# Optimization experiments

Hardware: AMD Instinct MI355X
Metric: run time of the kernel (lower is better)

## Reference

```python
import jax, jax.numpy as jnp
import numpy as np

EPS = 1e-5

def _conv1x1(x, w):
    # x: (B, Cin, N, K), w: (Cout, Cin) -> (B, Cout, N, K)
    return jnp.einsum('oc,bcnk->bonk', w, x)

def _bn2d(x, gamma, beta):
    # eval-mode BN with running_mean=0, running_var=1 (fresh init)
    scale = gamma / jnp.sqrt(1.0 + EPS)
    return x * scale[None, :, None, None] + beta[None, :, None, None]

def setup_inputs() -> dict:
    key = jax.random.key(0)
    ks = jax.random.split(key, 10)
    B, Cin, N, K = 8, 64, 1024, 32
    Cout, M = 64, 8
    Cin2 = 2 * Cin  # kernel_input='w_neighbor'
    features = jax.random.normal(ks[0], (B, Cin, N, K), dtype=jnp.float32)
    points_xyz = jax.random.normal(ks[1], (B, 3, N, K), dtype=jnp.float32)
    # ScoreNet convs: mlp_channels [7,16,16,16,M]; first 3 have BN (no bias), last has bias
    w1 = jax.random.normal(ks[2], (16, 7), dtype=jnp.float32) * (2.0 / 7) ** 0.5
    w2 = jax.random.normal(ks[3], (16, 16), dtype=jnp.float32) * (2.0 / 16) ** 0.5
    w3 = jax.random.normal(ks[4], (16, 16), dtype=jnp.float32) * (2.0 / 16) ** 0.5
    w4 = jax.random.normal(ks[5], (M, 16), dtype=jnp.float32) * (2.0 / 16) ** 0.5
    b4 = jnp.zeros((M,), dtype=jnp.float32)
    g1 = jnp.ones((16,), jnp.float32); be1 = jnp.zeros((16,), jnp.float32)
    g2 = jnp.ones((16,), jnp.float32); be2 = jnp.zeros((16,), jnp.float32)
    g3 = jnp.ones((16,), jnp.float32); be3 = jnp.zeros((16,), jnp.float32)
    # weight bank: kaiming_normal on (M, 2Cin, Cout) -> stored as (2Cin, M, Cout)
    wb = jax.random.normal(ks[6], (Cin2, M, Cout), dtype=jnp.float32) * (2.0 / Cin2) ** 0.5
    bn_g = jnp.ones((Cout,), jnp.float32); bn_b = jnp.zeros((Cout,), jnp.float32)
    return dict(features=features, points_xyz=points_xyz,
                w1=w1, g1=g1, be1=be1, w2=w2, g2=g2, be2=be2,
                w3=w3, g3=g3, be3=be3, w4=w4, b4=b4,
                weight_bank=wb, bn_g=bn_g, bn_b=bn_b)

def reference(features, points_xyz, w1, g1, be1, w2, g2, be2, w3, g3, be3,
              w4, b4, weight_bank, bn_g, bn_b):
    B, Cin, N, K = features.shape
    M = weight_bank.shape[1]
    # kernel_input = 'w_neighbor': concat(feat - center, feat) -> (B, 2Cin, N, K)
    center_f = features[..., :1]
    feat = jnp.concatenate([features - center_f, features], axis=1)
    # scorenet input = 'w_neighbor_dist': (center_xyz, xyz_diff, dist) -> (B, 7, N, K)
    center_xyz = jnp.broadcast_to(points_xyz[..., :1], points_xyz.shape)
    xyz_diff = points_xyz - center_xyz
    dist = jnp.sqrt(jnp.sum(xyz_diff * xyz_diff, axis=1, keepdims=True))
    xyz_feats = jnp.concatenate([center_xyz, xyz_diff, dist], axis=1)
    h = jax.nn.relu(_bn2d(_conv1x1(xyz_feats, w1), g1, be1))
    h = jax.nn.relu(_bn2d(_conv1x1(h, w2), g2, be2))
    h = jax.nn.relu(_bn2d(_conv1x1(h, w3), g3, be3))
    s = _conv1x1(h, w4) + b4[None, :, None, None]  # (B, M, N, K)
    scores = jax.nn.softmax(s, axis=1)
    scores = jnp.transpose(scores, (0, 2, 3, 1))  # (B, N, K, M)
    # matmul with weight bank then score-weighted sum over kernels, fused via einsum
    # original: (B,N,K,2Cin)@(2Cin,M*Cout) -> (B,N,K,M,Cout); sum_m scores * . -> (B,N,K,Cout)
    new_features = jnp.einsum('bcnk,cmo,bnkm->bonk', feat, weight_bank, scores)
    # BN2d (eval, fresh stats) + ReLU
    new_features = jax.nn.relu(_bn2d(new_features, bn_g, bn_b))
    return new_features
```

## Files before the change

### kernel.cpp

```cpp
#include <hip/hip_runtime.h>
#include <hip/hip_bf16.h>

typedef _Float16 f16;
typedef __attribute__((ext_vector_type(2))) _Float16 f16x2;
typedef __attribute__((ext_vector_type(8))) _Float16 f16x8;
typedef __attribute__((ext_vector_type(16))) float f32x16;

#define BNSCL 0.9999950000375f

__global__ __launch_bounds__(256) void k_scores(
    const float* __restrict__ xyz,
    const float* __restrict__ w1, const float* __restrict__ g1, const float* __restrict__ be1,
    const float* __restrict__ w2, const float* __restrict__ g2, const float* __restrict__ be2,
    const float* __restrict__ w3, const float* __restrict__ g3, const float* __restrict__ be3,
    const float* __restrict__ w4, const float* __restrict__ b4,
    const float* __restrict__ wb, f16* __restrict__ wbtA,
    f16* __restrict__ scores)
{
    const int tid = threadIdx.x;

    if (blockIdx.x < 256) {
        int idx = blockIdx.x * 256 + tid;
        int j    = idx & 7;
        int lane = (idx >> 3) & 63;
        int ks   = (idx >> 9) & 31;
        int bank = (idx >> 14) & 1;
        int ot   = idx >> 15;
        int c    = ks * 2 + (lane >> 5);
        int o    = ot * 32 + (lane & 31);
        float vD = wb[(c * 8 + j) * 64 + o];
        float v  = bank ? vD : vD + wb[((c + 64) * 8 + j) * 64 + o];
        wbtA[idx] = (f16)v;
    }

    float in7[2][7], h1[2][16], h2[2][16], s[2][8];

#pragma unroll
    for (int q = 0; q < 2; ++q) {
        int g = blockIdx.x * 512 + q * 256 + tid;
        int b = g >> 15;
        int p = g & 32767;
        int pc = p & ~31;
        const float* xb = xyz + (size_t)b * 98304;
        float cx = xb[pc], cy = xb[32768 + pc], cz = xb[65536 + pc];
        float dx = xb[p] - cx, dy = xb[32768 + p] - cy, dz = xb[65536 + p] - cz;
        in7[q][0] = cx; in7[q][1] = cy; in7[q][2] = cz;
        in7[q][3] = dx; in7[q][4] = dy; in7[q][5] = dz;
        in7[q][6] = sqrtf(dx * dx + dy * dy + dz * dz);
    }

#pragma unroll
    for (int o = 0; o < 16; ++o) {
        float a0 = 0.f, a1 = 0.f;
#pragma unroll
        for (int c = 0; c < 7; ++c) {
            float w = w1[o * 7 + c];
            a0 += w * in7[0][c]; a1 += w * in7[1][c];
        }
        float gs = g1[o] * BNSCL, bb = be1[o];
        h1[0][o] = fmaxf(a0 * gs + bb, 0.f);
        h1[1][o] = fmaxf(a1 * gs + bb, 0.f);
    }
#pragma unroll
    for (int o = 0; o < 16; ++o) {
        float a0 = 0.f, a1 = 0.f;
#pragma unroll
        for (int c = 0; c < 16; ++c) {
            float w = w2[o * 16 + c];
            a0 += w * h1[0][c]; a1 += w * h1[1][c];
        }
        float gs = g2[o] * BNSCL, bb = be2[o];
        h2[0][o] = fmaxf(a0 * gs + bb, 0.f);
        h2[1][o] = fmaxf(a1 * gs + bb, 0.f);
    }
#pragma unroll
    for (int o = 0; o < 16; ++o) {
        float a0 = 0.f, a1 = 0.f;
#pragma unroll
        for (int c = 0; c < 16; ++c) {
            float w = w3[o * 16 + c];
            a0 += w * h2[0][c]; a1 += w * h2[1][c];
        }
        float gs = g3[o] * BNSCL, bb = be3[o];
        h1[0][o] = fmaxf(a0 * gs + bb, 0.f);
        h1[1][o] = fmaxf(a1 * gs + bb, 0.f);
    }
#pragma unroll
    for (int o = 0; o < 8; ++o) {
        float bb = b4[o];
        float a0 = bb, a1 = bb;
#pragma unroll
        for (int c = 0; c < 16; ++c) {
            float w = w4[o * 16 + c];
            a0 += w * h1[0][c]; a1 += w * h1[1][c];
        }
        s[0][o] = a0; s[1][o] = a1;
    }

#pragma unroll
    for (int q = 0; q < 2; ++q) {
        int g = blockIdx.x * 512 + q * 256 + tid;
        float mx = s[q][0];
#pragma unroll
        for (int i = 1; i < 8; ++i) mx = fmaxf(mx, s[q][i]);
        float sum = 0.f;
#pragma unroll
        for (int i = 0; i < 8; ++i) { s[q][i] = __expf(s[q][i] - mx); sum += s[q][i]; }
        float inv = 1.f / sum;
        f16x8 o8;
#pragma unroll
        for (int i = 0; i < 8; ++i) o8[i] = (f16)(s[q][i] * inv);
        *(f16x8*)(scores + (size_t)g * 8) = o8;
    }
}

__global__ __launch_bounds__(1024) void k_g(
    const float* __restrict__ feat,
    const f16* __restrict__ wbtA,
    f16* __restrict__ Gt)
{
    __shared__ __align__(16) f16 ldsD[16384];
    __shared__ __align__(16) f16 gscr[16][512];

    const int tid  = threadIdx.x;
    const int lane = tid & 63;
    const int wave = tid >> 6;
    const int l31  = lane & 31;
    const int lh   = lane >> 5;

    const int ot     = blockIdx.x >> 8;
    const int window = (blockIdx.x & 255) * 16 + wave;
    const int ptglob = window * 64;
    const int b      = ptglob >> 15;
    const int ptb    = ptglob & 32767;
    const float* fb  = feat + (size_t)b * 2097152;

    const f16* src = wbtA + ot * 32768 + 16384;
#pragma unroll
    for (int it = 0; it < 2; ++it) {
        int idx = it * 1024 + tid;
        *(int4*)&ldsD[idx << 3] = *(const int4*)&src[idx << 3];
    }
    __syncthreads();

    const bool mon  = (l31 < 16);
    const int  mpos = l31 & 7;
    const f16x2 mk0 = { (f16)((mon && mpos == 0) ? 1.f : 0.f),
                        (f16)((mon && mpos == 1) ? 1.f : 0.f) };
    const f16x2 mk1 = { (f16)((mon && mpos == 2) ? 1.f : 0.f),
                        (f16)((mon && mpos == 3) ? 1.f : 0.f) };
    const f16x2 mk2 = { (f16)((mon && mpos == 4) ? 1.f : 0.f),
                        (f16)((mon && mpos == 5) ? 1.f : 0.f) };
    const f16x2 mk3 = { (f16)((mon && mpos == 6) ? 1.f : 0.f),
                        (f16)((mon && mpos == 7) ? 1.f : 0.f) };

    f32x16 accG = {};
    const f16* Ad = ldsD + (lane << 3);

#pragma unroll
    for (int kk = 0; kk < 32; ++kk) {
        f16x8 aD = *(const f16x8*)(Ad + ((size_t)kk << 9));
        const float* frow = fb + ((size_t)(2 * kk + lh) << 15) + ptb;
        float fcs = (l31 & 8) ? frow[32] : frow[0];
        f16 hC = (f16)(-fcs);
        f16x2 fg2 = {hC, hC};
        f16x2 q0 = mk0 * fg2, q1 = mk1 * fg2, q2 = mk2 * fg2, q3 = mk3 * fg2;
        f16x8 bG = {q0[0],q0[1],q1[0],q1[1],q2[0],q2[1],q3[0],q3[1]};
        accG = __builtin_amdgcn_mfma_f32_32x32x16_f16(aD, bG, accG, 0, 0, 0);
    }

    if (l31 < 16) {
        const int base = (l31 >> 3) * 256 + (l31 & 7);
#pragma unroll
        for (int r = 0; r < 16; ++r) {
            int o = (r & 3) + ((r >> 2) << 3) + (lh << 2);
            gscr[wave][base + o * 8] = (f16)accG[r];
        }
    }
    asm volatile("s_waitcnt lgkmcnt(0)" ::: "memory");
    __builtin_amdgcn_sched_barrier(0);
    {
        f16x8 gv = *(const f16x8*)&gscr[wave][lh * 256 + l31 * 8];
        size_t gg = (size_t)(window * 2 + lh);
        *(f16x8*)&Gt[(gg * 64 + ot * 32 + l31) * 8] = gv;
    }
}

__global__ __launch_bounds__(1024, 4) void k_main(
    const float* __restrict__ feat,
    const f16* __restrict__ scores,
    const f16* __restrict__ wbtA,
    const f16* __restrict__ Gt,
    const float* __restrict__ bn_g, const float* __restrict__ bn_b,
    float* __restrict__ out)
{
    __shared__ __align__(16) f16 lwb[16384];
    __shared__ __align__(16) float fbuf[8][2][1024];

    const int tid  = threadIdx.x;
    const int lane = tid & 63;
    const int wave = tid >> 6;
    const int l31  = lane & 31;
    const int lh   = lane >> 5;
    const int w64  = wave * 64;

    const int ot = blockIdx.x >> 8;
    const int g  = blockIdx.x & 255;
    const int pblock = g * 1024;
    const int b    = pblock >> 15;
    const int pt0  = (pblock & 32767) + w64;
    const int pc0  = pt0 + l31;
    const int pc1  = pc0 + 32;

    const float* fb = feat + (size_t)b * 2097152;
    const float* gsrc0 = fb + (pblock & 32767) + w64 + lane;

    const f16* src = wbtA + ot * 32768;
#pragma unroll
    for (int it = 0; it < 2; ++it) {
        int idx = it * 1024 + tid;
        *(int4*)&lwb[idx << 3] = *(const int4*)&src[idx << 3];
    }

    const int gpt = pblock + w64 + l31;
    f16x8 sv0 = *(const f16x8*)(scores + (size_t)gpt * 8);
    f16x8 sv1 = *(const f16x8*)(scores + (size_t)(gpt + 32) * 8);
    const f16x2 s0a = {sv0[0], sv0[1]}, s0b = {sv0[2], sv0[3]},
                s0c = {sv0[4], sv0[5]}, s0d = {sv0[6], sv0[7]};
    const f16x2 s1a = {sv1[0], sv1[1]}, s1b = {sv1[2], sv1[3]},
                s1c = {sv1[4], sv1[5]}, s1d = {sv1[6], sv1[7]};

    f32x16 acc0 = {}, acc1 = {};
    const f16* Alds = lwb + (lane << 3);

#define STAGE(t)                                                               \
    {                                                                          \
        __builtin_amdgcn_global_load_lds(                                      \
            (const __attribute__((address_space(1))) void*)                    \
                (gsrc0 + ((size_t)(2 * (t)) << 15)),                           \
            (__attribute__((address_space(3))) void*)&fbuf[(t) & 7][0][w64],   \
            4, 0, 0);                                                          \
        __builtin_amdgcn_global_load_lds(                                      \
            (const __attribute__((address_space(1))) void*)                    \
                (gsrc0 + ((size_t)(2 * (t) + 1) << 15)),                       \
            (__attribute__((address_space(3))) void*)&fbuf[(t) & 7][1][w64],   \
            4, 0, 0);                                                          \
    }

#define WAITV(n) asm volatile("s_waitcnt vmcnt(" #n ")" ::: "memory")

    __builtin_amdgcn_sched_barrier(0);
    STAGE(0); STAGE(1); STAGE(2); STAGE(3); STAGE(4); STAGE(5);

    asm volatile("s_waitcnt lgkmcnt(0)" ::: "memory");
    __builtin_amdgcn_s_barrier();

#define KSTEP(kk)                                                              \
    {                                                                          \
        f16x8 aS = *(const f16x8*)(Alds + ((size_t)(kk) << 9));                \
        const float* frow = fbuf[(kk) & 7][lh];                                \
        float fv0 = frow[w64 + l31], fv1 = frow[w64 + l31 + 32];               \
        f16 hR0 = (f16)fv0, hR1 = (f16)fv1;                                    \
        f16x2 fR0 = {hR0, hR0}, fR1 = {hR1, hR1};                              \
        f16x2 r0a = fR0 * s0a, r0b = fR0 * s0b, r0c = fR0 * s0c, r0d = fR0 * s0d; \
        f16x2 r1a = fR1 * s1a, r1b = fR1 * s1b, r1c = fR1 * s1c, r1d = fR1 * s1d; \
        f16x8 bS0 = {r0a[0],r0a[1],r0b[0],r0b[1],r0c[0],r0c[1],r0d[0],r0d[1]}; \
        f16x8 bS1 = {r1a[0],r1a[1],r1b[0],r1b[1],r1c[0],r1c[1],r1d[0],r1d[1]}; \
        acc0 = __builtin_amdgcn_mfma_f32_32x32x16_f16(aS, bS0, acc0, 0, 0, 0); \
        acc1 = __builtin_amdgcn_mfma_f32_32x32x16_f16(aS, bS1, acc1, 0, 0, 0); \
    }

#define PAIR(p)                                                                \
    STAGE(2 * (p) + 6) STAGE(2 * (p) + 7)                                      \
    WAITV(12);                                                                 \
    KSTEP(2 * (p)) KSTEP(2 * (p) + 1)

    PAIR(0)  PAIR(1)  PAIR(2)  PAIR(3)
    PAIR(4)  PAIR(5)  PAIR(6)  PAIR(7)
    PAIR(8)  PAIR(9)  PAIR(10) PAIR(11)
    PAIR(12)
    WAITV(8);
    KSTEP(26) KSTEP(27)
    WAITV(4);
    KSTEP(28) KSTEP(29)
    WAITV(0);
    KSTEP(30) KSTEP(31)
#undef PAIR
#undef KSTEP
#undef STAGE
#undef WAITV

    __builtin_amdgcn_sched_barrier(0);

    {
        const int g0 = (pblock + w64) >> 5;
        const f16x8 a2 = *(const f16x8*)
            &Gt[((size_t)(g0 + lh) * 64 + ot * 32 + l31) * 8];
        f16x8 z8 = {};
        f16x8 bC0 = lh ? z8 : sv0;
        f16x8 bC1 = lh ? sv1 : z8;
        acc0 = __builtin_amdgcn_mfma_f32_32x32x16_f16(a2, bC0, acc0, 0, 0, 0);
        acc1 = __builtin_amdgcn_mfma_f32_32x32x16_f16(a2, bC1, acc1, 0, 0, 0);
    }

#pragma unroll
    for (int r = 0; r < 16; ++r) {
        int o = ot * 32 + (r & 3) + ((r >> 2) << 3) + (lh << 2);
        float gs = bn_g[o] * BNSCL, bb = bn_b[o];
        size_t row = (size_t)(b * 64 + o) << 15;
        out[row + pc0] = fmaxf(acc0[r] * gs + bb, 0.f);
        out[row + pc1] = fmaxf(acc1[r] * gs + bb, 0.f);
    }
}

extern "C" void kernel_launch(void* const* d_in, const int* in_sizes, int n_in,
                              void* d_out, int out_size, void* d_ws, size_t ws_size,
                              hipStream_t stream)
{
    const float* features = (const float*)d_in[0];
    const float* xyz      = (const float*)d_in[1];
    const float* w1  = (const float*)d_in[2];
    const float* g1  = (const float*)d_in[3];
    const float* be1 = (const float*)d_in[4];
    const float* w2  = (const float*)d_in[5];
    const float* g2  = (const float*)d_in[6];
    const float* be2 = (const float*)d_in[7];
    const float* w3  = (const float*)d_in[8];
    const float* g3  = (const float*)d_in[9];
    const float* be3 = (const float*)d_in[10];
    const float* w4  = (const float*)d_in[11];
    const float* b4  = (const float*)d_in[12];
    const float* wb  = (const float*)d_in[13];
    const float* bn_g = (const float*)d_in[14];
    const float* bn_b = (const float*)d_in[15];

    f16* scores = (f16*)d_ws;
    f16* wbtA   = (f16*)((char*)d_ws + (4u << 20));
    f16* Gt     = (f16*)((char*)d_ws + (4u << 20) + 131072);

    k_scores<<<512, 256, 0, stream>>>(xyz, w1, g1, be1, w2, g2, be2,
                                      w3, g3, be3, w4, b4, wb, wbtA, scores);
    k_g<<<512, 1024, 0, stream>>>(features, wbtA, Gt);
    k_main<<<512, 1024, 0, stream>>>(features, scores, wbtA, Gt,
                                     bn_g, bn_b, (float*)d_out);
}
```

Baseline: 194.4 us.

## Merge score and center-feature kernels into one heterogeneous pre-pass launch

Combines k_scores and k_g into a single k_pre launch with 1280 blocks of 512 threads. The first 256 blocks compute the ScoreNet softmax scores, and the first 128 of those also write the transformed weight bank. The remaining 1024 blocks compute the center-feature term Gt, reading the weight bank directly from fp32 and converting it per block instead of depending on wbtA. This drops one kernel launch and the inter-kernel dependency, so both independent pre-computations can run concurrently. In exchange, each G block repeats the weight conversion with strided scalar loads, and LDS use is now allocated even for score blocks.

After: 188.6 us. 3.0% less time.

```diff
diff --git a/kernel.cpp b/kernel.cpp
--- a/kernel.cpp
+++ b/kernel.cpp
@@ -8,19 +8,96 @@
 
 #define BNSCL 0.9999950000375f
 
-__global__ __launch_bounds__(256) void k_scores(
+__global__ __launch_bounds__(512) void k_pre(
     const float* __restrict__ xyz,
     const float* __restrict__ w1, const float* __restrict__ g1, const float* __restrict__ be1,
     const float* __restrict__ w2, const float* __restrict__ g2, const float* __restrict__ be2,
     const float* __restrict__ w3, const float* __restrict__ g3, const float* __restrict__ be3,
     const float* __restrict__ w4, const float* __restrict__ b4,
     const float* __restrict__ wb, f16* __restrict__ wbtA,
+    const float* __restrict__ feat, f16* __restrict__ Gt,
     f16* __restrict__ scores)
 {
+    __shared__ __align__(16) f16 ldsD[16384];
+    __shared__ __align__(16) f16 gscr[8][512];
+
     const int tid = threadIdx.x;
-
-    if (blockIdx.x < 256) {
-        int idx = blockIdx.x * 256 + tid;
+    const int bx  = blockIdx.x;
+
+    if (bx >= 256) {
+        const int gb   = bx - 256;
+        const int ot   = gb >> 9;
+        const int lane = tid & 63;
+        const int wave = tid >> 6;
+        const int l31  = lane & 31;
+        const int lh   = lane >> 5;
+
+#pragma unroll
+        for (int it = 0; it < 4; ++it) {
+            int oct = it * 512 + tid;
+            int ln  = oct & 63;
+            int ks  = oct >> 6;
+            int c   = ks * 2 + (ln >> 5);
+            int o   = ot * 32 + (ln & 31);
+            f16x8 v;
+#pragma unroll
+            for (int j = 0; j < 8; ++j) v[j] = (f16)wb[(c * 8 + j) * 64 + o];
+            *(f16x8*)&ldsD[oct << 3] = v;
+        }
+        __syncthreads();
+
+        const int window = (gb & 511) * 8 + wave;
+        const int ptglob = window * 64;
+        const int b      = ptglob >> 15;
+        const int ptb    = ptglob & 32767;
+        const float* fb  = feat + (size_t)b * 2097152;
+
+        const bool mon  = (l31 < 16);
+        const int  mpos = l31 & 7;
+        const f16x2 mk0 = { (f16)((mon && mpos == 0) ? 1.f : 0.f),
+                            (f16)((mon && mpos == 1) ? 1.f : 0.f) };
+        const f16x2 mk1 = { (f16)((mon && mpos == 2) ? 1.f : 0.f),
+                            (f16)((mon && mpos == 3) ? 1.f : 0.f) };
+        const f16x2 mk2 = { (f16)((mon && mpos == 4) ? 1.f : 0.f),
+                            (f16)((mon && mpos == 5) ? 1.f : 0.f) };
+        const f16x2 mk3 = { (f16)((mon && mpos == 6) ? 1.f : 0.f),
+                            (f16)((mon && mpos == 7) ? 1.f : 0.f) };
+
+        f32x16 accG = {};
+        const f16* Ad = ldsD + (lane << 3);
+
+#pragma unroll
+        for (int kk = 0; kk < 32; ++kk) {
+            f16x8 aD = *(const f16x8*)(Ad + ((size_t)kk << 9));
+            const float* frow = fb + ((size_t)(2 * kk + lh) << 15) + ptb;
+            float fcs = (l31 & 8) ? frow[32] : frow[0];
+            f16 hC = (f16)(-fcs);
+            f16x2 fg2 = {hC, hC};
+            f16x2 q0 = mk0 * fg2, q1 = mk1 * fg2, q2 = mk2 * fg2, q3 = mk3 * fg2;
+            f16x8 bG = {q0[0],q0[1],q1[0],q1[1],q2[0],q2[1],q3[0],q3[1]};
+            accG = __builtin_amdgcn_mfma_f32_32x32x16_f16(aD, bG, accG, 0, 0, 0);
+        }
+
+        if (l31 < 16) {
+            const int base = (l31 >> 3) * 256 + (l31 & 7);
+#pragma unroll
+            for (int r = 0; r < 16; ++r) {
+                int o = (r & 3) + ((r >> 2) << 3) + (lh << 2);
+                gscr[wave][base + o * 8] = (f16)accG[r];
+            }
+        }
+        asm volatile("s_waitcnt lgkmcnt(0)" ::: "memory");
+        __builtin_amdgcn_sched_barrier(0);
+        {
+            f16x8 gv = *(const f16x8*)&gscr[wave][lh * 256 + l31 * 8];
+            size_t gg = (size_t)(window * 2 + lh);
+            *(f16x8*)&Gt[(gg * 64 + ot * 32 + l31) * 8] = gv;
+        }
+        return;
+    }
+
+    if (bx < 128) {
+        int idx = bx * 512 + tid;
         int j    = idx & 7;
         int lane = (idx >> 3) & 63;
         int ks   = (idx >> 9) & 31;
@@ -37,7 +114,7 @@
 
 #pragma unroll
     for (int q = 0; q < 2; ++q) {
-        int g = blockIdx.x * 512 + q * 256 + tid;
+        int g = bx * 1024 + q * 512 + tid;
         int b = g >> 15;
         int p = g & 32767;
         int pc = p & ~31;
@@ -99,7 +176,7 @@
 
 #pragma unroll
     for (int q = 0; q < 2; ++q) {
-        int g = blockIdx.x * 512 + q * 256 + tid;
+        int g = bx * 1024 + q * 512 + tid;
         float mx = s[q][0];
 #pragma unroll
         for (int i = 1; i < 8; ++i) mx = fmaxf(mx, s[q][i]);
@@ -111,78 +188,6 @@
 #pragma unroll
         for (int i = 0; i < 8; ++i) o8[i] = (f16)(s[q][i] * inv);
         *(f16x8*)(scores + (size_t)g * 8) = o8;
-    }
-}
-
-__global__ __launch_bounds__(1024) void k_g(
-    const float* __restrict__ feat,
-    const f16* __restrict__ wbtA,
-    f16* __restrict__ Gt)
-{
-    __shared__ __align__(16) f16 ldsD[16384];
-    __shared__ __align__(16) f16 gscr[16][512];
-
-    const int tid  = threadIdx.x;
-    const int lane = tid & 63;
-    const int wave = tid >> 6;
-    const int l31  = lane & 31;
-    const int lh   = lane >> 5;
-
-    const int ot     = blockIdx.x >> 8;
-    const int window = (blockIdx.x & 255) * 16 + wave;
-    const int ptglob = window * 64;
-    const int b      = ptglob >> 15;
-    const int ptb    = ptglob & 32767;
-    const float* fb  = feat + (size_t)b * 2097152;
-
-    const f16* src = wbtA + ot * 32768 + 16384;
-#pragma unroll
-    for (int it = 0; it < 2; ++it) {
-        int idx = it * 1024 + tid;
-        *(int4*)&ldsD[idx << 3] = *(const int4*)&src[idx << 3];
-    }
-    __syncthreads();
-
-    const bool mon  = (l31 < 16);
-    const int  mpos = l31 & 7;
-    const f16x2 mk0 = { (f16)((mon && mpos == 0) ? 1.f : 0.f),
-                        (f16)((mon && mpos == 1) ? 1.f : 0.f) };
-    const f16x2 mk1 = { (f16)((mon && mpos == 2) ? 1.f : 0.f),
-                        (f16)((mon && mpos == 3) ? 1.f : 0.f) };
-    const f16x2 mk2 = { (f16)((mon && mpos == 4) ? 1.f : 0.f),
-                        (f16)((mon && mpos == 5) ? 1.f : 0.f) };
-    const f16x2 mk3 = { (f16)((mon && mpos == 6) ? 1.f : 0.f),
-                        (f16)((mon && mpos == 7) ? 1.f : 0.f) };
-
-    f32x16 accG = {};
-    const f16* Ad = ldsD + (lane << 3);
-
-#pragma unroll
-    for (int kk = 0; kk < 32; ++kk) {
-        f16x8 aD = *(const f16x8*)(Ad + ((size_t)kk << 9));
-        const float* frow = fb + ((size_t)(2 * kk + lh) << 15) + ptb;
-        float fcs = (l31 & 8) ? frow[32] : frow[0];
-        f16 hC = (f16)(-fcs);
-        f16x2 fg2 = {hC, hC};
-        f16x2 q0 = mk0 * fg2, q1 = mk1 * fg2, q2 = mk2 * fg2, q3 = mk3 * fg2;
-        f16x8 bG = {q0[0],q0[1],q1[0],q1[1],q2[0],q2[1],q3[0],q3[1]};
-        accG = __builtin_amdgcn_mfma_f32_32x32x16_f16(aD, bG, accG, 0, 0, 0);
-    }
-
-    if (l31 < 16) {
-        const int base = (l31 >> 3) * 256 + (l31 & 7);
-#pragma unroll
-        for (int r = 0; r < 16; ++r) {
-            int o = (r & 3) + ((r >> 2) << 3) + (lh << 2);
-            gscr[wave][base + o * 8] = (f16)accG[r];
-        }
-    }
-    asm volatile("s_waitcnt lgkmcnt(0)" ::: "memory");
-    __builtin_amdgcn_sched_barrier(0);
-    {
-        f16x8 gv = *(const f16x8*)&gscr[wave][lh * 256 + l31 * 8];
-        size_t gg = (size_t)(window * 2 + lh);
-        *(f16x8*)&Gt[(gg * 64 + ot * 32 + l31) * 8] = gv;
     }
 }
 
@@ -338,9 +343,9 @@
     f16* wbtA   = (f16*)((char*)d_ws + (4u << 20));
     f16* Gt     = (f16*)((char*)d_ws + (4u << 20) + 131072);
 
-    k_scores<<<512, 256, 0, stream>>>(xyz, w1, g1, be1, w2, g2, be2,
-                                      w3, g3, be3, w4, b4, wb, wbtA, scores);
-    k_g<<<512, 1024, 0, stream>>>(features, wbtA, Gt);
+    k_pre<<<1280, 512, 0, stream>>>(xyz, w1, g1, be1, w2, g2, be2,
+                                    w3, g3, be3, w4, b4, wb, wbtA,
+                                    features, Gt, scores);
     k_main<<<512, 1024, 0, stream>>>(features, scores, wbtA, Gt,
                                      bn_g, bn_b, (float*)d_out);
 }
```
